# Kernel tuning notes

Measured on AMD Instinct MI355X. Metric: run time of the kernel, lower is better.

Reference implementation:

```python
import jax, jax.numpy as jnp
import numpy as np
import math

NUM_BUCKETS = 32
MAX_DISTANCE = 128

def _next_pow2(n):
    return 1 << (int(n) - 1).bit_length()

def _rel_pos_bucket(rel_pos):
    # causal T5 bucket: n = max(q - k, 0)
    n = jnp.maximum(-rel_pos, 0)
    max_exact = NUM_BUCKETS // 2
    is_small = n < max_exact
    n_safe = jnp.maximum(n, 1).astype(jnp.float32)
    val_if_large = max_exact + (
        jnp.log(n_safe / max_exact) / math.log(MAX_DISTANCE / max_exact) * (NUM_BUCKETS - max_exact)
    ).astype(jnp.int32)
    val_if_large = jnp.minimum(val_if_large, NUM_BUCKETS - 1)
    return jnp.where(is_small, n, val_if_large)

def setup_inputs() -> dict:
    key = jax.random.key(0)
    ks = jax.random.split(key, 20)
    B, L, D = 8, 2048, 128
    H, DQK, DV = 16, 64, 256
    s = 0.05
    return {
        'x': jax.random.normal(ks[0], (B, L, D), jnp.float32),
        'expansion': jax.random.normal(ks[1], (H, D), jnp.float32) * s,
        'reduction': jax.random.normal(ks[2], (H, D), jnp.float32) * s,
        'alphas': jax.random.normal(ks[3], (H,), jnp.float32),
        'dampen_factors': jax.random.normal(ks[4], (H,), jnp.float32),
        'rel_bias': jax.random.normal(ks[5], (NUM_BUCKETS, 1), jnp.float32) * s,
        'W_qk': jax.random.normal(ks[6], (D, DQK), jnp.float32) * s,
        'b_qk': jnp.zeros((DQK,), jnp.float32),
        'gamma': jax.random.normal(ks[7], (2, DQK), jnp.float32) * 0.02 + 1.0,
        'beta': jnp.zeros((2, DQK), jnp.float32),
        'W_v': jax.random.normal(ks[8], (D, DV), jnp.float32) * s,
        'b_v': jnp.zeros((DV,), jnp.float32),
        'W_reset': jax.random.normal(ks[9], (D, DV), jnp.float32) * s,
        'b_reset': jnp.zeros((DV,), jnp.float32),
        'W_update': jax.random.normal(ks[10], (D, D), jnp.float32) * s,
        'b_update': jnp.zeros((D,), jnp.float32),
        'Wh': jax.random.normal(ks[11], (D, D), jnp.float32) * s,
        'Uh': jax.random.normal(ks[12], (DV, D), jnp.float32) * s,
        'bh': jnp.zeros((D,), jnp.float32),
    }

def reference(x, expansion, reduction, alphas, dampen_factors, rel_bias,
              W_qk, b_qk, gamma, beta, W_v, b_v, W_reset, b_reset,
              W_update, b_update, Wh, Uh, bh):
    B, L, D = x.shape
    DQK = W_qk.shape[1]
    # ---- MultiHeadedEMA (causal, FFT conv) ----
    xe = jnp.einsum('bnd,hd->bnhd', x, expansion)  # [B,L,H,D]
    a = jax.nn.sigmoid(alphas)
    damp = jax.nn.sigmoid(dampen_factors)
    t = jnp.arange(L, dtype=x.dtype)
    kern = a[:, None] * ((1.0 - a) * damp)[:, None] ** t[None, :]  # [H,L]
    fft_len = _next_pow2(2 * L - 1)
    Xf = jnp.fft.rfft(xe, n=fft_len, axis=1)           # [B,F,H,D]
    Kf = jnp.fft.rfft(kern, n=fft_len, axis=-1)        # [H,F]
    y = jnp.fft.irfft(Xf * Kf.T[None, :, :, None], n=fft_len, axis=1)[:, :L]
    ema = jnp.einsum('bnhd,hd->bnd', y, reduction)     # [B,L,D]
    # ---- SingleHeadedAttention(ema, v_input=x) ----
    qk = jax.nn.silu(ema @ W_qk + b_qk)                # [B,L,DQK]
    q = qk * gamma[0] + beta[0]
    k = qk * gamma[1] + beta[1]
    v = jax.nn.silu(x @ W_v + b_v)                     # [B,L,DV]
    scale = D ** -0.5
    sim = jnp.einsum('bid,bjd->bij', q, k) * scale
    pos = jnp.arange(L)
    rel = pos[None, :] - pos[:, None]                  # [L,L] j - i
    bias = rel_bias[_rel_pos_bucket(rel), 0] * (DQK ** 0.5)
    sim = sim + bias
    sim = jnp.where(rel > 0, jnp.finfo(sim.dtype).min, sim)  # strict causal mask
    attn = jax.nn.softmax(sim, axis=-1)
    attn_out = jnp.einsum('bij,bjd->bid', attn, v)     # [B,L,DV]
    # ---- gating ----
    reset_gate = jax.nn.silu(ema @ W_reset + b_reset)
    update_gate = jax.nn.sigmoid(ema @ W_update + b_update)
    gated = attn_out * reset_gate
    Hh = jax.nn.silu(ema @ Wh + gated @ Uh + bh)
    return update_gate * Hh + (1.0 - update_gate) * x
```

## Files before the change

kernel.cpp:

```cpp
#include <hip/hip_runtime.h>
#include <hip/hip_bf16.h>
#include <math.h>

#define BB 8
#define LL 2048
#define DD 128
#define DQKN 64
#define DVN 256
#define MTOT (BB*LL)
#define SCALE 0.08838834764831845f
#define LOG2E 1.4426950408889634f
#define QSCALE (SCALE*LOG2E)

#define CHUNK 32
#define NCH (LL/CHUNK)
#define CT 4
#define NCHK 144

typedef __attribute__((ext_vector_type(4))) float f32x4;
typedef __attribute__((ext_vector_type(8))) short s16x8;

__device__ __forceinline__ float sigmoidf_(float x){ return 1.f/(1.f+__expf(-x)); }
__device__ __forceinline__ float siluf_(float x){ return x/(1.f+__expf(-x)); }
__device__ __forceinline__ __hip_bfloat16 f2bf(float f){ return __float2bfloat16(f); }
__device__ __forceinline__ ushort f2bfu(float f){ __hip_bfloat16 h = __float2bfloat16(f); return *(const ushort*)&h; }
__device__ __forceinline__ float bf2f(ushort u){ union{unsigned i; float f;} v; v.i = ((unsigned)u)<<16; return v.f; }

__device__ __forceinline__ void gl_lds16(const __hip_bfloat16* g, void* l) {
    __builtin_amdgcn_global_load_lds(
        (const __attribute__((address_space(1))) void*)g,
        (__attribute__((address_space(3))) void*)l, 16, 0, 0);
}

__global__ void pack_all(const float* __restrict__ Wqk, const float* __restrict__ Wv,
                         const float* __restrict__ Wrst, const float* __restrict__ Wu,
                         const float* __restrict__ Wh, const float* __restrict__ Uh,
                         const float* __restrict__ rel_bias,
                         __hip_bfloat16* __restrict__ WqkP, __hip_bfloat16* __restrict__ WvP,
                         __hip_bfloat16* __restrict__ WrstP, __hip_bfloat16* __restrict__ WuP,
                         __hip_bfloat16* __restrict__ WhP, __hip_bfloat16* __restrict__ UhP,
                         float* __restrict__ btab) {
    int blk = blockIdx.x;
    int l = threadIdx.x;
    if (blk == 272) {
        for (int n = l; n < LL; n += 64) {
            int bucket;
            if (n < 16) bucket = n;
            else {
                float v = logf((float)n * (1.0f/16.0f)) * (1.0f/logf(8.0f)) * 16.0f;
                bucket = 16 + (int)v;
                if (bucket > 31) bucket = 31;
            }
            btab[n] = rel_bias[bucket] * 8.0f * LOG2E;
        }
        return;
    }
    const float* W; __hip_bfloat16* Wp; int K, N;
    if (blk < 16)       { W=Wqk;  Wp=WqkP;  K=128; N=64; }
    else if (blk < 80)  { W=Wv;   Wp=WvP;   K=128; N=256; blk-=16; }
    else if (blk < 144) { W=Wrst; Wp=WrstP; K=128; N=256; blk-=80; }
    else if (blk < 176) { W=Wu;   Wp=WuP;   K=128; N=128; blk-=144; }
    else if (blk < 208) { W=Wh;   Wp=WhP;   K=128; N=128; blk-=176; }
    else                { W=Uh;   Wp=UhP;   K=256; N=128; blk-=208; }
    int k32 = blk % (K/32), n16 = blk / (K/32);
    int col = n16*16 + (l & 15);
    int krow = k32*32 + (l >> 4)*8;
    ushort tmp[8];
    #pragma unroll
    for (int j = 0; j < 8; ++j) tmp[j] = f2bfu(W[(size_t)(krow + j)*N + col]);
    *reinterpret_cast<uint4*>(Wp + ((size_t)blk*64 + l)*8) = *reinterpret_cast<uint4*>(tmp);
}

__global__ __launch_bounds__(256) void ema_scanA(const float* __restrict__ x,
                                                 const float* __restrict__ alphas,
                                                 const float* __restrict__ damps,
                                                 float* __restrict__ sl) {
    int tid = blockIdx.x * 256 + threadIdx.x;
    int d = tid & 127;
    int c = (tid >> 7) & (NCH - 1);
    int b = tid >> 13;
    float u[16], r[16];
    #pragma unroll
    for (int h = 0; h < 16; ++h) {
        float a = sigmoidf_(alphas[h]);
        r[h] = (1.f - a) * sigmoidf_(damps[h]);
        u[h] = 0.f;
    }
    const float* xp = x + ((size_t)b * LL + c * CHUNK) * DD + d;
    #pragma unroll 4
    for (int i = 0; i < CHUNK; ++i) {
        float xv = xp[(size_t)i * DD];
        #pragma unroll
        for (int h = 0; h < 16; ++h) u[h] = fmaf(r[h], u[h], xv);
    }
    float* slp = sl + ((size_t)b * NCH + c) * 16 * DD + d;
    #pragma unroll
    for (int h = 0; h < 16; ++h) slp[(size_t)h * DD] = u[h];
}

__global__ __launch_bounds__(256) void ema_scanB(const float* __restrict__ alphas,
                                                 const float* __restrict__ damps,
                                                 const float* __restrict__ sl,
                                                 float* __restrict__ carry) {
    int tid = blockIdx.x * 256 + threadIdx.x;
    int d = tid & 127;
    int h = (tid >> 7) & 15;
    int b = tid >> 11;
    float a = sigmoidf_(alphas[h]);
    float r = (1.f - a) * sigmoidf_(damps[h]);
    float rC = r;
    #pragma unroll
    for (int q = 0; q < 5; ++q) rC *= rC;
    const float* slp = sl + ((size_t)b * NCH * 16 + h) * DD + d;
    float* cp = carry + ((size_t)b * NCH * 16 + h) * DD + d;
    float u = 0.f;
    for (int c = 0; c < NCH; ++c) {
        cp[(size_t)c * 16 * DD] = u;
        u = slp[(size_t)c * 16 * DD] + rC * u;
    }
}

__global__ __launch_bounds__(256) void ema_scanC(const float* __restrict__ x,
                                                 const float* __restrict__ expansion,
                                                 const float* __restrict__ reduction,
                                                 const float* __restrict__ alphas,
                                                 const float* __restrict__ damps,
                                                 const float* __restrict__ carry,
                                                 __hip_bfloat16* __restrict__ emab,
                                                 __hip_bfloat16* __restrict__ xb) {
    int tid = blockIdx.x * 256 + threadIdx.x;
    int d = tid & 127;
    int c = (tid >> 7) & (NCH - 1);
    int b = tid >> 13;
    float u[16], r[16], we[16];
    #pragma unroll
    for (int h = 0; h < 16; ++h) {
        float a = sigmoidf_(alphas[h]);
        r[h] = (1.f - a) * sigmoidf_(damps[h]);
        we[h] = reduction[h * DD + d] * a * expansion[h * DD + d];
        u[h] = carry[((size_t)b * NCH + c) * 16 * DD + (size_t)h * DD + d];
    }
    const float* xp = x + ((size_t)b * LL + c * CHUNK) * DD + d;
    __hip_bfloat16* ep = emab + ((size_t)b * LL + c * CHUNK) * DD + d;
    __hip_bfloat16* xbp = xb + ((size_t)b * LL + c * CHUNK) * DD + d;
    #pragma unroll 4
    for (int i = 0; i < CHUNK; ++i) {
        float xv = xp[(size_t)i * DD];
        float acc = 0.f;
        #pragma unroll
        for (int h = 0; h < 16; ++h) {
            u[h] = fmaf(r[h], u[h], xv);
            acc = fmaf(we[h], u[h], acc);
        }
        ep[(size_t)i * DD] = f2bf(acc);
        xbp[(size_t)i * DD] = f2bf(xv);
    }
}

__global__ __launch_bounds__(256) void gemm_qk(const __hip_bfloat16* __restrict__ A,
        const __hip_bfloat16* __restrict__ Wp, const float* __restrict__ bias,
        const float* __restrict__ gamma, const float* __restrict__ beta,
        __hip_bfloat16* __restrict__ qb, __hip_bfloat16* __restrict__ kb) {
    __shared__ char AsB[64*256];
    const int row0 = blockIdx.x * 64;
    const int t = threadIdx.x, w = t>>6, lane = t&63, l16 = lane&15, l4 = lane>>4;
    #pragma unroll
    for (int p = 0; p < 4; ++p) {
        int idx = p*256 + t;
        int row = idx / 16, u = idx % 16;
        uint4 d = *reinterpret_cast<const uint4*>(A + (size_t)(row0+row)*DD + u*8);
        *reinterpret_cast<uint4*>(AsB + row*256 + ((u*16) ^ ((row&7)<<4))) = d;
    }
    __syncthreads();
    f32x4 acc[4];
    #pragma unroll
    for (int n = 0; n < 4; ++n) acc[n] = (f32x4){0.f,0.f,0.f,0.f};
    const int arow = w*16 + l16;
    #pragma unroll
    for (int k32 = 0; k32 < 4; ++k32) {
        s16x8 af = *reinterpret_cast<const s16x8*>(AsB + arow*256 + ((k32*64 + l4*16) ^ ((arow&7)<<4)));
        #pragma unroll
        for (int n = 0; n < 4; ++n) {
            s16x8 bfr = *reinterpret_cast<const s16x8*>(Wp + ((size_t)(n*4 + k32)*64 + lane)*8);
            acc[n] = __builtin_amdgcn_mfma_f32_16x16x32_bf16(af, bfr, acc[n], 0, 0, 0);
        }
    }
    #pragma unroll
    for (int n = 0; n < 4; ++n) {
        int col = n*16 + l16;
        float bb = bias[col];
        float g0 = gamma[col], g1 = gamma[DQKN + col];
        float be0 = beta[col], be1 = beta[DQKN + col];
        #pragma unroll
        for (int r = 0; r < 4; ++r) {
            int row = w*16 + l4*4 + r;
            float s = siluf_(acc[n][r] + bb);
            qb[(size_t)(row0+row)*DQKN + col] = f2bf((s*g0 + be0) * QSCALE);
            kb[(size_t)(row0+row)*DQKN + col] = f2bf(s*g1 + be1);
        }
    }
}

__global__ __launch_bounds__(256) void gemm_vrst(const __hip_bfloat16* __restrict__ xb,
        const __hip_bfloat16* __restrict__ emab,
        const __hip_bfloat16* __restrict__ WvP, const __hip_bfloat16* __restrict__ WrstP,
        const float* __restrict__ b_v, const float* __restrict__ b_rst,
        __hip_bfloat16* __restrict__ vT, __hip_bfloat16* __restrict__ rstb) {
    __shared__ char AsB[64*256];
    const int mode = blockIdx.y;
    const __hip_bfloat16* A = mode ? emab : xb;
    const __hip_bfloat16* Wp = mode ? WrstP : WvP;
    const float* bias = mode ? b_rst : b_v;
    const int row0 = blockIdx.x * 64;
    const int t = threadIdx.x, w = t>>6, lane = t&63, l16 = lane&15, l4 = lane>>4;
    #pragma unroll
    for (int p = 0; p < 4; ++p) {
        int idx = p*256 + t;
        int row = idx / 16, u = idx % 16;
        uint4 d = *reinterpret_cast<const uint4*>(A + (size_t)(row0+row)*DD + u*8);
        *reinterpret_cast<uint4*>(AsB + row*256 + ((u*16) ^ ((row&7)<<4))) = d;
    }
    __syncthreads();
    f32x4 acc[16];
    #pragma unroll
    for (int n = 0; n < 16; ++n) acc[n] = (f32x4){0.f,0.f,0.f,0.f};
    const int arow = w*16 + l16;
    #pragma unroll
    for (int k32 = 0; k32 < 4; ++k32) {
        s16x8 af = *reinterpret_cast<const s16x8*>(AsB + arow*256 + ((k32*64 + l4*16) ^ ((arow&7)<<4)));
        #pragma unroll
        for (int n = 0; n < 16; ++n) {
            s16x8 bfr = *reinterpret_cast<const s16x8*>(Wp + ((size_t)(n*4 + k32)*64 + lane)*8);
            acc[n] = __builtin_amdgcn_mfma_f32_16x16x32_bf16(af, bfr, acc[n], 0, 0, 0);
        }
    }
    if (mode == 0) {
        int bb_i = row0 >> 11;
        int lpos0 = (row0 & 2047) + w*16 + l4*4;
        #pragma unroll
        for (int n = 0; n < 16; ++n) {
            int col = n*16 + l16;
            float bb = bias[col];
            ushort pk[4];
            #pragma unroll
            for (int r = 0; r < 4; ++r) pk[r] = f2bfu(siluf_(acc[n][r] + bb));
            *reinterpret_cast<ushort4*>(vT + ((size_t)bb_i*DVN + col)*LL + lpos0) = *reinterpret_cast<ushort4*>(pk);
        }
    } else {
        #pragma unroll
        for (int n = 0; n < 16; ++n) {
            int col = n*16 + l16;
            float bb = bias[col];
            #pragma unroll
            for (int r = 0; r < 4; ++r) {
                int row = w*16 + l4*4 + r;
                rstb[(size_t)(row0+row)*DVN + col] = f2bf(siluf_(acc[n][r] + bb));
            }
        }
    }
}

__global__ __launch_bounds__(256) void attn_kernel(
    const __hip_bfloat16* __restrict__ qg, const __hip_bfloat16* __restrict__ kg,
    const __hip_bfloat16* __restrict__ vTg, const float* __restrict__ btab,
    __hip_bfloat16* __restrict__ aob, __hip_bfloat16* __restrict__ part_o,
    float* __restrict__ part_ml) {
    __shared__ __hip_bfloat16 Ks[64 * 64];
    __shared__ __hip_bfloat16 Vs[256 * 64];
    __shared__ __hip_bfloat16 Ps[4][16][72];
    __shared__ float btl[320];
    const int cid = NCHK - 1 - (int)blockIdx.x;
    const int b = blockIdx.y;
    int g = 0;
    while (cid >= 2*(g+1)*(g+2)) ++g;
    const int rel = cid - 2*g*(g+1);
    const int ti = 4*g + rel/(g+1);
    const int cch = rel % (g+1);
    const int i0 = ti * 64;
    const int jlo = cch * (CT*64);
    int jhi = jlo + CT*64; { int je = (ti+1)*64; if (jhi > je) jhi = je; }
    const int nt = (jhi - jlo) >> 6;
    const int t = threadIdx.x;
    const int w = t >> 6, lane = t & 63;
    const int l16 = lane & 15, l4 = lane >> 4;
    char* KsB = (char*)Ks;
    char* VsB = (char*)Vs;

    int dmin = i0 - jhi + 1; if (dmin < 0) dmin = 0;
    const int cnt = (i0 + 63 - jlo) - dmin + 1;
    for (int idx = t; idx < cnt; idx += 256) btl[idx] = btab[dmin + idx];

    const int irow = i0 + w * 16 + l16;
    s16x8 qf[2];
    qf[0] = *reinterpret_cast<const s16x8*>(qg + ((size_t)b * LL + irow) * DQKN + l4 * 8);
    qf[1] = *reinterpret_cast<const s16x8*>(qg + ((size_t)b * LL + irow) * DQKN + 32 + l4 * 8);

    f32x4 o[16];
    #pragma unroll
    for (int n16 = 0; n16 < 16; ++n16) o[n16] = (f32x4){0.f, 0.f, 0.f, 0.f};
    float m[4] = {-1e30f, -1e30f, -1e30f, -1e30f};
    float l[4] = {0.f, 0.f, 0.f, 0.f};

    for (int tt = 0; tt < nt; ++tt) {
        const int j0 = jlo + tt * 64;
        __syncthreads();
        #pragma unroll
        for (int i = 0; i < 2; ++i) {
            int base = w * 128 + i * 64;
            int idx = base + lane;
            int row = idx >> 3;
            int c16 = (idx & 7) ^ (row & 7);
            gl_lds16(kg + ((size_t)b * LL + j0 + row) * DQKN + c16 * 8, KsB + base * 16);
        }
        #pragma unroll
        for (int i = 0; i < 8; ++i) {
            int base = w * 512 + i * 64;
            int idx = base + lane;
            int n = idx >> 3;
            int c16 = (idx & 7) ^ (n & 7);
            gl_lds16(vTg + ((size_t)b * DVN + n) * LL + j0 + c16 * 8, VsB + base * 16);
        }
        __syncthreads();
        f32x4 s[4];
        #pragma unroll
        for (int t16 = 0; t16 < 4; ++t16) s[t16] = (f32x4){0.f, 0.f, 0.f, 0.f};
        #pragma unroll
        for (int c = 0; c < 2; ++c) {
            #pragma unroll
            for (int t16 = 0; t16 < 4; ++t16) {
                int j = t16 * 16 + l16;
                s16x8 kf = *reinterpret_cast<const s16x8*>(KsB + j * 128 + ((c * 64 + l4 * 16) ^ ((j & 7) << 4)));
                s[t16] = __builtin_amdgcn_mfma_f32_16x16x32_bf16(qf[c], kf, s[t16], 0, 0, 0);
            }
        }
        float sv[4][4];
        float rmax[4] = {-1e30f, -1e30f, -1e30f, -1e30f};
        #pragma unroll
        for (int t16 = 0; t16 < 4; ++t16) {
            #pragma unroll
            for (int r = 0; r < 4; ++r) {
                int row = l4 * 4 + r;
                int dlt = (i0 + w * 16 + row) - (j0 + t16 * 16 + l16);
                int bi = dlt - dmin; if (bi < 0) bi = 0;
                float bv = btl[bi];
                float val = (dlt >= 0) ? (s[t16][r] + bv) : -1e30f;
                sv[t16][r] = val;
                rmax[r] = fmaxf(rmax[r], val);
            }
        }
        #pragma unroll
        for (int off = 1; off < 16; off <<= 1) {
            #pragma unroll
            for (int r = 0; r < 4; ++r) rmax[r] = fmaxf(rmax[r], __shfl_xor(rmax[r], off));
        }
        bool need = (rmax[0] > m[0]) || (rmax[1] > m[1]) || (rmax[2] > m[2]) || (rmax[3] > m[3]);
        if (__any(need)) {
            float alpha[4];
            #pragma unroll
            for (int r = 0; r < 4; ++r) {
                float mn = fmaxf(m[r], rmax[r]);
                alpha[r] = exp2f(m[r] - mn);
                m[r] = mn;
                l[r] *= alpha[r];
            }
            #pragma unroll
            for (int n16 = 0; n16 < 16; ++n16) {
                #pragma unroll
                for (int r = 0; r < 4; ++r) o[n16][r] *= alpha[r];
            }
        }
        float psum[4] = {0.f, 0.f, 0.f, 0.f};
        #pragma unroll
        for (int t16 = 0; t16 < 4; ++t16) {
            #pragma unroll
            for (int r = 0; r < 4; ++r) {
                float p = exp2f(sv[t16][r] - m[r]);
                psum[r] += p;
                Ps[w][l4 * 4 + r][t16 * 16 + l16] = f2bf(p);
            }
        }
        #pragma unroll
        for (int off = 1; off < 16; off <<= 1) {
            #pragma unroll
            for (int r = 0; r < 4; ++r) psum[r] += __shfl_xor(psum[r], off);
        }
        #pragma unroll
        for (int r = 0; r < 4; ++r) l[r] += psum[r];
        #pragma unroll
        for (int c = 0; c < 2; ++c) {
            s16x8 pf = *reinterpret_cast<const s16x8*>(&Ps[w][l16][c * 32 + l4 * 8]);
            #pragma unroll
            for (int n16 = 0; n16 < 16; ++n16) {
                int n = n16 * 16 + l16;
                s16x8 vf = *reinterpret_cast<const s16x8*>(VsB + n * 128 + ((c * 64 + l4 * 16) ^ ((n & 7) << 4)));
                o[n16] = __builtin_amdgcn_mfma_f32_16x16x32_bf16(pf, vf, o[n16], 0, 0, 0);
            }
        }
    }
    if (ti < 4) {
        float invl[4];
        #pragma unroll
        for (int r = 0; r < 4; ++r) invl[r] = 1.f / l[r];
        #pragma unroll
        for (int n16 = 0; n16 < 16; ++n16) {
            #pragma unroll
            for (int r = 0; r < 4; ++r) {
                aob[((size_t)b * LL + i0 + w * 16 + l4 * 4 + r) * DVN + n16 * 16 + l16] = f2bf(o[n16][r] * invl[r]);
            }
        }
    } else {
        const size_t slot = (size_t)b * NCHK + cid;
        __hip_bfloat16* po = part_o + slot * (64 * 256);
        #pragma unroll
        for (int n16 = 0; n16 < 16; ++n16) {
            #pragma unroll
            for (int r = 0; r < 4; ++r)
                po[(size_t)(w * 16 + l4 * 4 + r) * 256 + n16 * 16 + l16] = f2bf(o[n16][r]);
        }
        if (l16 == 0) {
            #pragma unroll
            for (int r = 0; r < 4; ++r) {
                int row = w * 16 + l4 * 4 + r;
                part_ml[slot * 128 + row * 2]     = m[r];
                part_ml[slot * 128 + row * 2 + 1] = l[r];
            }
        }
    }
}

__global__ __launch_bounds__(256) void attn_combine(const __hip_bfloat16* __restrict__ part_o,
                                                    const float* __restrict__ part_ml,
                                                    __hip_bfloat16* __restrict__ aob) {
    const int ti = 4 + (int)blockIdx.x;
    const int ch = blockIdx.y;
    const int b = blockIdx.z;
    const int g = ti >> 2;
    const int nc = g + 1;
    const int cid0 = 2*g*(g+1) + (ti - 4*g)*(g+1);
    const size_t slot0 = (size_t)b * NCHK + cid0;
    __shared__ float sW[8][64];
    __shared__ float sinvL[64];
    const int t = threadIdx.x;
    if (t < 64) {
        float M = -1e30f;
        for (int c = 0; c < nc; ++c)
            M = fmaxf(M, part_ml[(slot0 + c) * 128 + t * 2]);
        float L = 0.f;
        for (int c = 0; c < nc; ++c) {
            float wv = exp2f(part_ml[(slot0 + c) * 128 + t * 2] - M);
            sW[c][t] = wv;
            L += wv * part_ml[(slot0 + c) * 128 + t * 2 + 1];
        }
        sinvL[t] = 1.f / L;
    }
    __syncthreads();
    const int i0 = ti * 64;
    #pragma unroll
    for (int it = 0; it < 4; ++it) {
        int idx = it * 256 + t;
        int row = idx >> 4, c8 = idx & 15;
        int colu = ch * 16 + c8;
        float acc[8] = {0.f,0.f,0.f,0.f,0.f,0.f,0.f,0.f};
        for (int c = 0; c < nc; ++c) {
            float wv = sW[c][row];
            uint4 d = *reinterpret_cast<const uint4*>(part_o + (slot0 + c) * (size_t)(64*256) + row * 256 + colu * 8);
            const ushort* pp = (const ushort*)&d;
            #pragma unroll
            for (int j = 0; j < 8; ++j) acc[j] = fmaf(wv, bf2f(pp[j]), acc[j]);
        }
        float il = sinvL[row];
        ushort pk[8];
        #pragma unroll
        for (int j = 0; j < 8; ++j) pk[j] = f2bfu(acc[j] * il);
        *reinterpret_cast<uint4*>(aob + ((size_t)b * LL + i0 + row) * DVN + colu * 8) = *reinterpret_cast<uint4*>(pk);
    }
}

__global__ __launch_bounds__(256) void final_mfma(
        const __hip_bfloat16* __restrict__ emab, const __hip_bfloat16* __restrict__ aob,
        const __hip_bfloat16* __restrict__ rstb, const float* __restrict__ x,
        const __hip_bfloat16* __restrict__ WhP, const __hip_bfloat16* __restrict__ UhP,
        const __hip_bfloat16* __restrict__ WuP, const float* __restrict__ bh,
        const float* __restrict__ bu, float* __restrict__ out) {
    __shared__ char As1[64*256];
    __shared__ char As2[64*512];
    const int row0 = blockIdx.x * 64;
    const int ch = blockIdx.y;
    const int t = threadIdx.x, w = t>>6, lane = t&63, l16 = lane&15, l4 = lane>>4;
    #pragma unroll
    for (int p = 0; p < 4; ++p) {
        int idx = p*256 + t;
        int row = idx / 16, u = idx % 16;
        uint4 d = *reinterpret_cast<const uint4*>(emab + (size_t)(row0+row)*DD + u*8);
        *reinterpret_cast<uint4*>(As1 + row*256 + ((u*16) ^ ((row&7)<<4))) = d;
    }
    #pragma unroll
    for (int p = 0; p < 8; ++p) {
        int idx = p*256 + t;
        int row = idx / 32, u = idx % 32;
        uint4 da = *reinterpret_cast<const uint4*>(aob + (size_t)(row0+row)*DVN + u*8);
        uint4 dr = *reinterpret_cast<const uint4*>(rstb + (size_t)(row0+row)*DVN + u*8);
        const ushort* pa = (const ushort*)&da;
        const ushort* pr = (const ushort*)&dr;
        ushort gg[8];
        #pragma unroll
        for (int j = 0; j < 8; ++j) gg[j] = f2bfu(bf2f(pa[j]) * bf2f(pr[j]));
        *reinterpret_cast<uint4*>(As2 + row*512 + ((u*16) ^ ((row&7)<<4))) = *reinterpret_cast<uint4*>(gg);
    }
    __syncthreads();
    f32x4 acc1[4], acc2[4];
    #pragma unroll
    for (int n = 0; n < 4; ++n) { acc1[n] = (f32x4){0.f,0.f,0.f,0.f}; acc2[n] = (f32x4){0.f,0.f,0.f,0.f}; }
    const int arow = w*16 + l16;
    #pragma unroll
    for (int k32 = 0; k32 < 4; ++k32) {
        s16x8 af = *reinterpret_cast<const s16x8*>(As1 + arow*256 + ((k32*64 + l4*16) ^ ((arow&7)<<4)));
        #pragma unroll
        for (int n = 0; n < 4; ++n) {
            s16x8 bw = *reinterpret_cast<const s16x8*>(WhP + ((size_t)((ch*4+n)*4 + k32)*64 + lane)*8);
            acc1[n] = __builtin_amdgcn_mfma_f32_16x16x32_bf16(af, bw, acc1[n], 0, 0, 0);
            s16x8 bu2 = *reinterpret_cast<const s16x8*>(WuP + ((size_t)((ch*4+n)*4 + k32)*64 + lane)*8);
            acc2[n] = __builtin_amdgcn_mfma_f32_16x16x32_bf16(af, bu2, acc2[n], 0, 0, 0);
        }
    }
    #pragma unroll
    for (int k32 = 0; k32 < 8; ++k32) {
        s16x8 gf = *reinterpret_cast<const s16x8*>(As2 + arow*512 + ((k32*64 + l4*16) ^ ((arow&7)<<4)));
        #pragma unroll
        for (int n = 0; n < 4; ++n) {
            s16x8 bw = *reinterpret_cast<const s16x8*>(UhP + ((size_t)((ch*4+n)*8 + k32)*64 + lane)*8);
            acc1[n] = __builtin_amdgcn_mfma_f32_16x16x32_bf16(gf, bw, acc1[n], 0, 0, 0);
        }
    }
    #pragma unroll
    for (int n = 0; n < 4; ++n) {
        int col = ch*64 + n*16 + l16;
        float bbh = bh[col], bbu = bu[col];
        #pragma unroll
        for (int r = 0; r < 4; ++r) {
            int row = w*16 + l4*4 + r;
            size_t gidx = (size_t)(row0+row)*DD + col;
            float hh = siluf_(acc1[n][r] + bbh);
            float u = sigmoidf_(acc2[n][r] + bbu);
            float xv = x[gidx];
            out[gidx] = u*hh + (1.f-u)*xv;
        }
    }
}

extern "C" void kernel_launch(void* const* d_in, const int* in_sizes, int n_in,
                              void* d_out, int out_size, void* d_ws, size_t ws_size,
                              hipStream_t stream) {
    const float* x        = (const float*)d_in[0];
    const float* expansion= (const float*)d_in[1];
    const float* reduction= (const float*)d_in[2];
    const float* alphas   = (const float*)d_in[3];
    const float* damps    = (const float*)d_in[4];
    const float* rel_bias = (const float*)d_in[5];
    const float* W_qk     = (const float*)d_in[6];
    const float* b_qk     = (const float*)d_in[7];
    const float* gamma    = (const float*)d_in[8];
    const float* beta     = (const float*)d_in[9];
    const float* W_v      = (const float*)d_in[10];
    const float* b_v      = (const float*)d_in[11];
    const float* W_reset  = (const float*)d_in[12];
    const float* b_reset  = (const float*)d_in[13];
    const float* W_update = (const float*)d_in[14];
    const float* b_update = (const float*)d_in[15];
    const float* Wh       = (const float*)d_in[16];
    const float* Uh       = (const float*)d_in[17];
    const float* bh       = (const float*)d_in[18];
    float* out = (float*)d_out;

    char* base = (char*)d_ws;
    __hip_bfloat16* emab = (__hip_bfloat16*)base;  base += (size_t)MTOT * DD * 2;
    __hip_bfloat16* xb   = (__hip_bfloat16*)base;  base += (size_t)MTOT * DD * 2;
    __hip_bfloat16* qb   = (__hip_bfloat16*)base;  base += (size_t)MTOT * DQKN * 2;
    __hip_bfloat16* kb   = (__hip_bfloat16*)base;  base += (size_t)MTOT * DQKN * 2;
    __hip_bfloat16* vT   = (__hip_bfloat16*)base;  base += (size_t)MTOT * DVN * 2;
    __hip_bfloat16* rstb = (__hip_bfloat16*)base;  base += (size_t)MTOT * DVN * 2;
    __hip_bfloat16* aob  = (__hip_bfloat16*)base;  base += (size_t)MTOT * DVN * 2;
    float* btab  = (float*)base;                   base += (size_t)LL * 4;
    float* sl    = (float*)base;                   base += (size_t)BB * NCH * 16 * DD * 4;
    float* carry = (float*)base;                   base += (size_t)BB * NCH * 16 * DD * 4;
    __hip_bfloat16* WqkP = (__hip_bfloat16*)base;  base += (size_t)DD * DQKN * 2;
    __hip_bfloat16* WvP  = (__hip_bfloat16*)base;  base += (size_t)DD * DVN * 2;
    __hip_bfloat16* WrstP= (__hip_bfloat16*)base;  base += (size_t)DD * DVN * 2;
    __hip_bfloat16* WuP  = (__hip_bfloat16*)base;  base += (size_t)DD * DD * 2;
    __hip_bfloat16* WhP  = (__hip_bfloat16*)base;  base += (size_t)DD * DD * 2;
    __hip_bfloat16* UhP  = (__hip_bfloat16*)base;  base += (size_t)DVN * DD * 2;
    __hip_bfloat16* part_o = (__hip_bfloat16*)base; base += (size_t)BB * NCHK * 64 * 256 * 2;
    float* part_ml = (float*)base;                 base += (size_t)BB * NCHK * 128 * 4;

    pack_all<<<273, 64, 0, stream>>>(W_qk, W_v, W_reset, W_update, Wh, Uh, rel_bias,
                                     WqkP, WvP, WrstP, WuP, WhP, UhP, btab);

    ema_scanA<<<BB * NCH * DD / 256, 256, 0, stream>>>(x, alphas, damps, sl);
    ema_scanB<<<BB * 16 * DD / 256, 256, 0, stream>>>(alphas, damps, sl, carry);
    ema_scanC<<<BB * NCH * DD / 256, 256, 0, stream>>>(x, expansion, reduction, alphas, damps, carry, emab, xb);

    gemm_qk<<<MTOT/64, 256, 0, stream>>>(emab, WqkP, b_qk, gamma, beta, qb, kb);
    gemm_vrst<<<dim3(MTOT/64, 2), 256, 0, stream>>>(xb, emab, WvP, WrstP, b_v, b_reset, vT, rstb);

    attn_kernel<<<dim3(NCHK, BB), 256, 0, stream>>>(qb, kb, vT, btab, aob, part_o, part_ml);
    attn_combine<<<dim3(28, 2, BB), 256, 0, stream>>>(part_o, part_ml, aob);

    final_mfma<<<dim3(MTOT/64, 2), 256, 0, stream>>>(emab, aob, rstb, x, WhP, UhP, WuP, bh, b_update, out);
}
```

Before: 120.9 us.

## Fuse QK and V/reset GEMMs, move bf16 x cast into scanA, reorder attention grid

```diff
diff --git a/kernel.cpp b/kernel.cpp
--- a/kernel.cpp
+++ b/kernel.cpp
@@ -74,7 +74,8 @@
 __global__ __launch_bounds__(256) void ema_scanA(const float* __restrict__ x,
                                                  const float* __restrict__ alphas,
                                                  const float* __restrict__ damps,
-                                                 float* __restrict__ sl) {
+                                                 float* __restrict__ sl,
+                                                 __hip_bfloat16* __restrict__ xb) {
     int tid = blockIdx.x * 256 + threadIdx.x;
     int d = tid & 127;
     int c = (tid >> 7) & (NCH - 1);
@@ -87,9 +88,11 @@
         u[h] = 0.f;
     }
     const float* xp = x + ((size_t)b * LL + c * CHUNK) * DD + d;
+    __hip_bfloat16* xbp = xb + ((size_t)b * LL + c * CHUNK) * DD + d;
     #pragma unroll 4
     for (int i = 0; i < CHUNK; ++i) {
         float xv = xp[(size_t)i * DD];
+        xbp[(size_t)i * DD] = f2bf(xv);
         #pragma unroll
         for (int h = 0; h < 16; ++h) u[h] = fmaf(r[h], u[h], xv);
     }
@@ -114,20 +117,20 @@
     const float* slp = sl + ((size_t)b * NCH * 16 + h) * DD + d;
     float* cp = carry + ((size_t)b * NCH * 16 + h) * DD + d;
     float u = 0.f;
+    #pragma unroll 8
     for (int c = 0; c < NCH; ++c) {
         cp[(size_t)c * 16 * DD] = u;
         u = slp[(size_t)c * 16 * DD] + rC * u;
     }
 }
 
-__global__ __launch_bounds__(256) void ema_scanC(const float* __restrict__ x,
+__global__ __launch_bounds__(256) void ema_scanC(const __hip_bfloat16* __restrict__ xb,
                                                  const float* __restrict__ expansion,
                                                  const float* __restrict__ reduction,
                                                  const float* __restrict__ alphas,
                                                  const float* __restrict__ damps,
                                                  const float* __restrict__ carry,
-                                                 __hip_bfloat16* __restrict__ emab,
-                                                 __hip_bfloat16* __restrict__ xb) {
+                                                 __hip_bfloat16* __restrict__ emab) {
     int tid = blockIdx.x * 256 + threadIdx.x;
     int d = tid & 127;
     int c = (tid >> 7) & (NCH - 1);
@@ -140,12 +143,11 @@
         we[h] = reduction[h * DD + d] * a * expansion[h * DD + d];
         u[h] = carry[((size_t)b * NCH + c) * 16 * DD + (size_t)h * DD + d];
     }
-    const float* xp = x + ((size_t)b * LL + c * CHUNK) * DD + d;
+    const __hip_bfloat16* xp = xb + ((size_t)b * LL + c * CHUNK) * DD + d;
     __hip_bfloat16* ep = emab + ((size_t)b * LL + c * CHUNK) * DD + d;
-    __hip_bfloat16* xbp = xb + ((size_t)b * LL + c * CHUNK) * DD + d;
     #pragma unroll 4
     for (int i = 0; i < CHUNK; ++i) {
-        float xv = xp[(size_t)i * DD];
+        float xv = __bfloat162float(xp[(size_t)i * DD]);
         float acc = 0.f;
         #pragma unroll
         for (int h = 0; h < 16; ++h) {
@@ -153,15 +155,21 @@
             acc = fmaf(we[h], u[h], acc);
         }
         ep[(size_t)i * DD] = f2bf(acc);
-        xbp[(size_t)i * DD] = f2bf(xv);
-    }
-}
-
-__global__ __launch_bounds__(256) void gemm_qk(const __hip_bfloat16* __restrict__ A,
-        const __hip_bfloat16* __restrict__ Wp, const float* __restrict__ bias,
-        const float* __restrict__ gamma, const float* __restrict__ beta,
+    }
+}
+
+__global__ __launch_bounds__(256) void gemm_fused(const __hip_bfloat16* __restrict__ xb,
+        const __hip_bfloat16* __restrict__ emab,
+        const __hip_bfloat16* __restrict__ WvP, const __hip_bfloat16* __restrict__ WrstP,
+        const __hip_bfloat16* __restrict__ WqkP,
+        const float* __restrict__ b_v, const float* __restrict__ b_rst,
+        const float* __restrict__ b_qk, const float* __restrict__ gamma,
+        const float* __restrict__ beta,
+        __hip_bfloat16* __restrict__ vT, __hip_bfloat16* __restrict__ rstb,
         __hip_bfloat16* __restrict__ qb, __hip_bfloat16* __restrict__ kb) {
     __shared__ char AsB[64*256];
+    const int mode = blockIdx.y;
+    const __hip_bfloat16* A = (mode == 0) ? xb : emab;
     const int row0 = blockIdx.x * 64;
     const int t = threadIdx.x, w = t>>6, lane = t&63, l16 = lane&15, l4 = lane>>4;
     #pragma unroll
@@ -172,59 +180,41 @@
         *reinterpret_cast<uint4*>(AsB + row*256 + ((u*16) ^ ((row&7)<<4))) = d;
     }
     __syncthreads();
-    f32x4 acc[4];
-    #pragma unroll
-    for (int n = 0; n < 4; ++n) acc[n] = (f32x4){0.f,0.f,0.f,0.f};
     const int arow = w*16 + l16;
-    #pragma unroll
-    for (int k32 = 0; k32 < 4; ++k32) {
-        s16x8 af = *reinterpret_cast<const s16x8*>(AsB + arow*256 + ((k32*64 + l4*16) ^ ((arow&7)<<4)));
+    if (mode == 2) {
+        f32x4 acc[4];
+        #pragma unroll
+        for (int n = 0; n < 4; ++n) acc[n] = (f32x4){0.f,0.f,0.f,0.f};
+        #pragma unroll
+        for (int k32 = 0; k32 < 4; ++k32) {
+            s16x8 af = *reinterpret_cast<const s16x8*>(AsB + arow*256 + ((k32*64 + l4*16) ^ ((arow&7)<<4)));
+            #pragma unroll
+            for (int n = 0; n < 4; ++n) {
+                s16x8 bfr = *reinterpret_cast<const s16x8*>(WqkP + ((size_t)(n*4 + k32)*64 + lane)*8);
+                acc[n] = __builtin_amdgcn_mfma_f32_16x16x32_bf16(af, bfr, acc[n], 0, 0, 0);
+            }
+        }
         #pragma unroll
         for (int n = 0; n < 4; ++n) {
-            s16x8 bfr = *reinterpret_cast<const s16x8*>(Wp + ((size_t)(n*4 + k32)*64 + lane)*8);
-            acc[n] = __builtin_amdgcn_mfma_f32_16x16x32_bf16(af, bfr, acc[n], 0, 0, 0);
-        }
-    }
-    #pragma unroll
-    for (int n = 0; n < 4; ++n) {
-        int col = n*16 + l16;
-        float bb = bias[col];
-        float g0 = gamma[col], g1 = gamma[DQKN + col];
-        float be0 = beta[col], be1 = beta[DQKN + col];
-        #pragma unroll
-        for (int r = 0; r < 4; ++r) {
-            int row = w*16 + l4*4 + r;
-            float s = siluf_(acc[n][r] + bb);
-            qb[(size_t)(row0+row)*DQKN + col] = f2bf((s*g0 + be0) * QSCALE);
-            kb[(size_t)(row0+row)*DQKN + col] = f2bf(s*g1 + be1);
-        }
-    }
-}
-
-__global__ __launch_bounds__(256) void gemm_vrst(const __hip_bfloat16* __restrict__ xb,
-        const __hip_bfloat16* __restrict__ emab,
-        const __hip_bfloat16* __restrict__ WvP, const __hip_bfloat16* __restrict__ WrstP,
-        const float* __restrict__ b_v, const float* __restrict__ b_rst,
-        __hip_bfloat16* __restrict__ vT, __hip_bfloat16* __restrict__ rstb) {
-    __shared__ char AsB[64*256];
-    const int mode = blockIdx.y;
-    const __hip_bfloat16* A = mode ? emab : xb;
+            int col = n*16 + l16;
+            float bb = b_qk[col];
+            float g0 = gamma[col], g1 = gamma[DQKN + col];
+            float be0 = beta[col], be1 = beta[DQKN + col];
+            #pragma unroll
+            for (int r = 0; r < 4; ++r) {
+                int row = w*16 + l4*4 + r;
+                float s = siluf_(acc[n][r] + bb);
+                qb[(size_t)(row0+row)*DQKN + col] = f2bf((s*g0 + be0) * QSCALE);
+                kb[(size_t)(row0+row)*DQKN + col] = f2bf(s*g1 + be1);
+            }
+        }
+        return;
+    }
     const __hip_bfloat16* Wp = mode ? WrstP : WvP;
     const float* bias = mode ? b_rst : b_v;
-    const int row0 = blockIdx.x * 64;
-    const int t = threadIdx.x, w = t>>6, lane = t&63, l16 = lane&15, l4 = lane>>4;
-    #pragma unroll
-    for (int p = 0; p < 4; ++p) {
-        int idx = p*256 + t;
-        int row = idx / 16, u = idx % 16;
-        uint4 d = *reinterpret_cast<const uint4*>(A + (size_t)(row0+row)*DD + u*8);
-        *reinterpret_cast<uint4*>(AsB + row*256 + ((u*16) ^ ((row&7)<<4))) = d;
-    }
-    __syncthreads();
     f32x4 acc[16];
     #pragma unroll
     for (int n = 0; n < 16; ++n) acc[n] = (f32x4){0.f,0.f,0.f,0.f};
-    const int arow = w*16 + l16;
     #pragma unroll
     for (int k32 = 0; k32 < 4; ++k32) {
         s16x8 af = *reinterpret_cast<const s16x8*>(AsB + arow*256 + ((k32*64 + l4*16) ^ ((arow&7)<<4)));
@@ -269,8 +259,8 @@
     __shared__ __hip_bfloat16 Vs[256 * 64];
     __shared__ __hip_bfloat16 Ps[4][16][72];
     __shared__ float btl[320];
-    const int cid = NCHK - 1 - (int)blockIdx.x;
-    const int b = blockIdx.y;
+    const int cid = NCHK - 1 - (int)blockIdx.y;
+    const int b = blockIdx.x;
     int g = 0;
     while (cid >= 2*(g+1)*(g+2)) ++g;
     const int rel = cid - 2*g*(g+1);
@@ -595,14 +585,15 @@
     pack_all<<<273, 64, 0, stream>>>(W_qk, W_v, W_reset, W_update, Wh, Uh, rel_bias,
                                      WqkP, WvP, WrstP, WuP, WhP, UhP, btab);
 
-    ema_scanA<<<BB * NCH * DD / 256, 256, 0, stream>>>(x, alphas, damps, sl);
+    ema_scanA<<<BB * NCH * DD / 256, 256, 0, stream>>>(x, alphas, damps, sl, xb);
     ema_scanB<<<BB * 16 * DD / 256, 256, 0, stream>>>(alphas, damps, sl, carry);
-    ema_scanC<<<BB * NCH * DD / 256, 256, 0, stream>>>(x, expansion, reduction, alphas, damps, carry, emab, xb);
-
-    gemm_qk<<<MTOT/64, 256, 0, stream>>>(emab, WqkP, b_qk, gamma, beta, qb, kb);
-    gemm_vrst<<<dim3(MTOT/64, 2), 256, 0, stream>>>(xb, emab, WvP, WrstP, b_v, b_reset, vT, rstb);
-
-    attn_kernel<<<dim3(NCHK, BB), 256, 0, stream>>>(qb, kb, vT, btab, aob, part_o, part_ml);
+    ema_scanC<<<BB * NCH * DD / 256, 256, 0, stream>>>(xb, expansion, reduction, alphas, damps, carry, emab);
+
+    gemm_fused<<<dim3(MTOT/64, 3), 256, 0, stream>>>(xb, emab, WvP, WrstP, WqkP,
+                                                     b_v, b_reset, b_qk, gamma, beta,
+                                                     vT, rstb, qb, kb);
+
+    attn_kernel<<<dim3(BB, NCHK), 256, 0, stream>>>(qb, kb, vT, btab, aob, part_o, part_ml);
     attn_combine<<<dim3(28, 2, BB), 256, 0, stream>>>(part_o, part_ml, aob);
 
     final_mfma<<<dim3(MTOT/64, 2), 256, 0, stream>>>(emab, aob, rstb, x, WhP, UhP, WuP, bh, b_update, out);
```

New measurement: 117.8 us (median of 3 runs). 2.6% less time.
